# Kernel tuning notes

Measured on AMD Instinct MI355X. Metric: run time of the kernel, lower is better.

The kernel has to match this reference:

```python
import jax, jax.numpy as jnp
import numpy as np

N_NODES = 100000
N_EDGES = 2000000
H = 128


def setup_inputs() -> dict:
    key = jax.random.key(0)
    ks = jax.random.split(key, 5)
    z_src = jax.random.normal(ks[0], (N_NODES, H), dtype=jnp.float32)
    z_dst = jax.random.normal(ks[1], (N_NODES, H), dtype=jnp.float32)
    edge_label_index = jax.random.randint(ks[2], (2, N_EDGES), 0, N_NODES, dtype=jnp.int64)
    # Linear(2H, H) and Linear(H, 1) params (stored as [in, out] for x @ W)
    W1 = jax.random.normal(ks[3], (2 * H, H), dtype=jnp.float32) * (1.0 / np.sqrt(2 * H))
    b1 = jnp.zeros((H,), dtype=jnp.float32)
    W2 = jax.random.normal(ks[4], (H, 1), dtype=jnp.float32) * (1.0 / np.sqrt(H))
    b2 = jnp.zeros((1,), dtype=jnp.float32)
    return {"z_src": z_src, "z_dst": z_dst, "edge_label_index": edge_label_index,
            "W1": W1, "b1": b1, "W2": W2, "b2": b2}


def reference(z_src, z_dst, edge_label_index, W1, b1, W2, b2):
    row, col = edge_label_index[0], edge_label_index[1]
    # gather + concat -> [E, 2H]
    z = jnp.concatenate([z_src[row], z_dst[col]], axis=-1)
    h = jax.nn.relu(z @ W1 + b1)          # [E, H]
    out = h @ W2 + b2                     # [E, 1]
    return out.reshape(-1)
```

## Files before the change

kernel.cpp:

```cpp
#include <hip/hip_runtime.h>

#define HDIM 128

__device__ __forceinline__ unsigned short f2bf_rne(float f) {
    unsigned int u = __float_as_uint(f);
    u += 0x7fffu + ((u >> 16) & 1u);
    return (unsigned short)(u >> 16);
}

__global__ __launch_bounds__(256) void node_gemm_dual(
    const float* __restrict__ Zs, const float* __restrict__ Zd,
    const float* __restrict__ W1, const float* __restrict__ b1,
    unsigned short* __restrict__ Abuf, unsigned short* __restrict__ Bbuf,
    int M, int gb)
{
    __shared__ float zT[128][36];
    __shared__ float ws[64][128];

    const bool second = (blockIdx.x >= gb);
    const float* __restrict__ Z    = second ? Zd : Zs;
    const float* __restrict__ W    = second ? (W1 + HDIM * HDIM) : W1;
    unsigned short* __restrict__ C = second ? Bbuf : Abuf;
    const int bx   = second ? (blockIdx.x - gb) : blockIdx.x;
    const int t    = threadIdx.x;
    const int row0 = bx * 32;

    {
        const int r  = t >> 3;
        const int k0 = (t & 7) << 4;
        int rg = row0 + r;
        if (rg >= M) rg = M - 1;
        const float4* Zv = reinterpret_cast<const float4*>(Z + (size_t)rg * HDIM + k0);
        float4 v0 = Zv[0], v1 = Zv[1], v2 = Zv[2], v3 = Zv[3];
        float vv[16] = {v0.x,v0.y,v0.z,v0.w, v1.x,v1.y,v1.z,v1.w,
                        v2.x,v2.y,v2.z,v2.w, v3.x,v3.y,v3.z,v3.w};
        #pragma unroll
        for (int i = 0; i < 16; ++i) zT[k0 + i][r] = vv[i];
    }

    const int tx = t & 31;
    const int ty = t >> 5;

    float acc[4][4];
    if (second) {
        const float4 bv = *reinterpret_cast<const float4*>(b1 + tx * 4);
        #pragma unroll
        for (int r = 0; r < 4; ++r) {
            acc[r][0] = bv.x; acc[r][1] = bv.y; acc[r][2] = bv.z; acc[r][3] = bv.w;
        }
    } else {
        #pragma unroll
        for (int r = 0; r < 4; ++r)
            #pragma unroll
            for (int c = 0; c < 4; ++c) acc[r][c] = 0.f;
    }

    for (int kk = 0; kk < 128; kk += 64) {
        __syncthreads();
        {
            const float4* Wv = reinterpret_cast<const float4*>(W + (size_t)kk * HDIM);
            float4* Sv = reinterpret_cast<float4*>(&ws[0][0]);
            #pragma unroll
            for (int i = 0; i < 8; ++i) Sv[t + 256 * i] = Wv[t + 256 * i];
        }
        __syncthreads();

        #pragma unroll 8
        for (int k = 0; k < 64; ++k) {
            const float4 zv = *reinterpret_cast<const float4*>(&zT[kk + k][ty * 4]);
            const float4 wv = *reinterpret_cast<const float4*>(&ws[k][tx * 4]);
            acc[0][0] += zv.x * wv.x; acc[0][1] += zv.x * wv.y;
            acc[0][2] += zv.x * wv.z; acc[0][3] += zv.x * wv.w;
            acc[1][0] += zv.y * wv.x; acc[1][1] += zv.y * wv.y;
            acc[1][2] += zv.y * wv.z; acc[1][3] += zv.y * wv.w;
            acc[2][0] += zv.z * wv.x; acc[2][1] += zv.z * wv.y;
            acc[2][2] += zv.z * wv.z; acc[2][3] += zv.z * wv.w;
            acc[3][0] += zv.w * wv.x; acc[3][1] += zv.w * wv.y;
            acc[3][2] += zv.w * wv.z; acc[3][3] += zv.w * wv.w;
        }
    }

    #pragma unroll
    for (int r = 0; r < 4; ++r) {
        const int row = row0 + ty * 4 + r;
        if (row < M) {
            ushort4 o;
            o.x = f2bf_rne(acc[r][0]); o.y = f2bf_rne(acc[r][1]);
            o.z = f2bf_rne(acc[r][2]); o.w = f2bf_rne(acc[r][3]);
            *reinterpret_cast<ushort4*>(C + (size_t)row * HDIM + tx * 4) = o;
        }
    }
}

__global__ __launch_bounds__(256) void edge_decode_bf16(
    const unsigned short* __restrict__ A, const unsigned short* __restrict__ Bm,
    const int* __restrict__ idx,
    const float* __restrict__ W2, const float* __restrict__ b2,
    float* __restrict__ out, int E)
{
    const int t   = threadIdx.x;
    const int sub = t & 15;
    const int grp = t >> 4;

    float w2r[8];
    #pragma unroll
    for (int i = 0; i < 8; ++i) w2r[i] = W2[sub * 8 + i];
    const float b2s = b2[0];

    const int stride = gridDim.x * 16;
    for (int e = blockIdx.x * 16 + grp; e < E; e += stride) {
        const int r = idx[e];
        const int c = idx[E + e];
        const uint4 av = *reinterpret_cast<const uint4*>(A  + (size_t)r * HDIM + sub * 8);
        const uint4 bv = *reinterpret_cast<const uint4*>(Bm + (size_t)c * HDIM + sub * 8);

        float s = 0.f;
        #pragma unroll
        for (int i = 0; i < 4; ++i) {
            const unsigned int ua = (&av.x)[i];
            const unsigned int ub = (&bv.x)[i];
            const float a0 = __uint_as_float(ua << 16);
            const float a1 = __uint_as_float(ua & 0xffff0000u);
            const float b0 = __uint_as_float(ub << 16);
            const float b1v = __uint_as_float(ub & 0xffff0000u);
            s += fmaxf(a0 + b0,  0.f) * w2r[2 * i];
            s += fmaxf(a1 + b1v, 0.f) * w2r[2 * i + 1];
        }
        s += __shfl_xor(s, 1);
        s += __shfl_xor(s, 2);
        s += __shfl_xor(s, 4);
        s += __shfl_xor(s, 8);
        if (sub == 0) out[e] = s + b2s;
    }
}

extern "C" void kernel_launch(void* const* d_in, const int* in_sizes, int n_in,
                              void* d_out, int out_size, void* d_ws, size_t ws_size,
                              hipStream_t stream)
{
    const float* z_src = (const float*)d_in[0];
    const float* z_dst = (const float*)d_in[1];
    const int*   eidx  = (const int*)d_in[2];
    const float* W1    = (const float*)d_in[3];
    const float* b1    = (const float*)d_in[4];
    const float* W2    = (const float*)d_in[5];
    const float* b2    = (const float*)d_in[6];
    float*       outp  = (float*)d_out;

    const int Nn = in_sizes[0] / HDIM;
    const int E  = in_sizes[2] / 2;

    unsigned short* Abuf = (unsigned short*)d_ws;
    unsigned short* Bbuf = Abuf + (size_t)Nn * HDIM;

    const int gb = (Nn + 31) / 32;
    node_gemm_dual<<<2 * gb, 256, 0, stream>>>(z_src, z_dst, W1, b1, Abuf, Bbuf, Nn, gb);
    edge_decode_bf16<<<8192, 256, 0, stream>>>(Abuf, Bbuf, eidx, W2, b2, outp, E);
}
```

Baseline: 339.2 us.

## Use bf16 MFMA for node projection GEMM and unroll edge decode by two

Replaces the fp32 FMA node GEMM with a bf16 MFMA (16x16x32) kernel. A small pre-kernel converts and transposes W1 to bf16, and Z tiles are converted to bf16 in shared memory. The edge decode loop now handles two edges per iteration so more gather loads are in flight. This adds an extra kernel launch and bf16 rounding of the inputs, which lowers precision. The output stores become scalar 2-byte writes that may coalesce poorly.

```diff
diff --git a/kernel.cpp b/kernel.cpp
--- a/kernel.cpp
+++ b/kernel.cpp
@@ -1,93 +1,104 @@
 #include <hip/hip_runtime.h>
 
 #define HDIM 128
+
+typedef __bf16 bf16_t;
+typedef bf16_t bf16x8 __attribute__((ext_vector_type(8)));
+typedef float  f32x4  __attribute__((ext_vector_type(4)));
 
 __device__ __forceinline__ unsigned short f2bf_rne(float f) {
     unsigned int u = __float_as_uint(f);
     u += 0x7fffu + ((u >> 16) & 1u);
     return (unsigned short)(u >> 16);
 }
+__device__ __forceinline__ unsigned int pk_bf2(float a, float b) {
+    return (unsigned int)f2bf_rne(a) | ((unsigned int)f2bf_rne(b) << 16);
+}
 
-__global__ __launch_bounds__(256) void node_gemm_dual(
+__global__ __launch_bounds__(256) void convert_w1(
+    const float* __restrict__ W1, unsigned short* __restrict__ Wt)
+{
+    const int o = blockIdx.x * 256 + threadIdx.x;
+    const int g = o >> 14, rem = o & 16383, n = rem >> 7, k = rem & 127;
+    Wt[o] = f2bf_rne(W1[g * 16384 + k * 128 + n]);
+}
+
+#define ZP 136
+__global__ __launch_bounds__(256) void node_gemm_mfma(
     const float* __restrict__ Zs, const float* __restrict__ Zd,
-    const float* __restrict__ W1, const float* __restrict__ b1,
+    const unsigned short* __restrict__ Wt, const float* __restrict__ b1,
     unsigned short* __restrict__ Abuf, unsigned short* __restrict__ Bbuf,
     int M, int gb)
 {
-    __shared__ float zT[128][36];
-    __shared__ float ws[64][128];
+    __shared__ unsigned short zs[64 * ZP];
+    __shared__ unsigned short wsm[128 * ZP];
 
     const bool second = (blockIdx.x >= gb);
-    const float* __restrict__ Z    = second ? Zd : Zs;
-    const float* __restrict__ W    = second ? (W1 + HDIM * HDIM) : W1;
-    unsigned short* __restrict__ C = second ? Bbuf : Abuf;
+    const float* __restrict__ Z          = second ? Zd : Zs;
+    const unsigned short* __restrict__ W = Wt + (second ? 128 * 128 : 0);
+    unsigned short* __restrict__ C       = second ? Bbuf : Abuf;
     const int bx   = second ? (blockIdx.x - gb) : blockIdx.x;
+    const int row0 = bx * 64;
     const int t    = threadIdx.x;
-    const int row0 = bx * 32;
 
-    {
-        const int r  = t >> 3;
-        const int k0 = (t & 7) << 4;
-        int rg = row0 + r;
-        if (rg >= M) rg = M - 1;
-        const float4* Zv = reinterpret_cast<const float4*>(Z + (size_t)rg * HDIM + k0);
-        float4 v0 = Zv[0], v1 = Zv[1], v2 = Zv[2], v3 = Zv[3];
-        float vv[16] = {v0.x,v0.y,v0.z,v0.w, v1.x,v1.y,v1.z,v1.w,
-                        v2.x,v2.y,v2.z,v2.w, v3.x,v3.y,v3.z,v3.w};
+    #pragma unroll
+    for (int j = 0; j < 8; ++j) {
+        const int u   = t + 256 * j;
+        const int row = u >> 5;
+        const int c4  = u & 31;
+        int rg = row0 + row; if (rg >= M) rg = M - 1;
+        const float4 v = *reinterpret_cast<const float4*>(Z + (size_t)rg * HDIM + c4 * 4);
+        uint2 p; p.x = pk_bf2(v.x, v.y); p.y = pk_bf2(v.z, v.w);
+        *reinterpret_cast<uint2*>(zs + row * ZP + c4 * 4) = p;
+    }
+    #pragma unroll
+    for (int j = 0; j < 8; ++j) {
+        const int u  = t + 256 * j;
+        const int n  = u >> 4;
+        const int k8 = u & 15;
+        const uint4 v = *reinterpret_cast<const uint4*>(W + n * 128 + k8 * 8);
+        *reinterpret_cast<uint4*>(wsm + n * ZP + k8 * 8) = v;
+    }
+    __syncthreads();
+
+    const int lane = t & 63;
+    const int wave = t >> 6;
+    const int m    = lane & 15;
+    const int quad = lane >> 4;
+    const int rw   = wave & 1;
+    const int cw   = wave >> 1;
+
+    const int aoff0 = (rw * 32 +  0 + m) * ZP + quad * 8;
+    const int aoff1 = (rw * 32 + 16 + m) * ZP + quad * 8;
+    const int boff  = (cw * 64 + m) * ZP + quad * 8;
+
+    f32x4 acc[2][4] = {};
+    #pragma unroll
+    for (int ks = 0; ks < 4; ++ks) {
+        const int ko = ks * 32;
+        const bf16x8 a0 = *reinterpret_cast<const bf16x8*>(zs + aoff0 + ko);
+        const bf16x8 a1 = *reinterpret_cast<const bf16x8*>(zs + aoff1 + ko);
         #pragma unroll
-        for (int i = 0; i < 16; ++i) zT[k0 + i][r] = vv[i];
-    }
-
-    const int tx = t & 31;
-    const int ty = t >> 5;
-
-    float acc[4][4];
-    if (second) {
-        const float4 bv = *reinterpret_cast<const float4*>(b1 + tx * 4);
-        #pragma unroll
-        for (int r = 0; r < 4; ++r) {
-            acc[r][0] = bv.x; acc[r][1] = bv.y; acc[r][2] = bv.z; acc[r][3] = bv.w;
-        }
-    } else {
-        #pragma unroll
-        for (int r = 0; r < 4; ++r)
-            #pragma unroll
-            for (int c = 0; c < 4; ++c) acc[r][c] = 0.f;
-    }
-
-    for (int kk = 0; kk < 128; kk += 64) {
-        __syncthreads();
-        {
-            const float4* Wv = reinterpret_cast<const float4*>(W + (size_t)kk * HDIM);
-            float4* Sv = reinterpret_cast<float4*>(&ws[0][0]);
-            #pragma unroll
-            for (int i = 0; i < 8; ++i) Sv[t + 256 * i] = Wv[t + 256 * i];
-        }
-        __syncthreads();
-
-        #pragma unroll 8
-        for (int k = 0; k < 64; ++k) {
-            const float4 zv = *reinterpret_cast<const float4*>(&zT[kk + k][ty * 4]);
-            const float4 wv = *reinterpret_cast<const float4*>(&ws[k][tx * 4]);
-            acc[0][0] += zv.x * wv.x; acc[0][1] += zv.x * wv.y;
-            acc[0][2] += zv.x * wv.z; acc[0][3] += zv.x * wv.w;
-            acc[1][0] += zv.y * wv.x; acc[1][1] += zv.y * wv.y;
-            acc[1][2] += zv.y * wv.z; acc[1][3] += zv.y * wv.w;
-            acc[2][0] += zv.z * wv.x; acc[2][1] += zv.z * wv.y;
-            acc[2][2] += zv.z * wv.z; acc[2][3] += zv.z * wv.w;
-            acc[3][0] += zv.w * wv.x; acc[3][1] += zv.w * wv.y;
-            acc[3][2] += zv.w * wv.z; acc[3][3] += zv.w * wv.w;
+        for (int ct = 0; ct < 4; ++ct) {
+            const bf16x8 bb = *reinterpret_cast<const bf16x8*>(wsm + boff + ct * 16 * ZP + ko);
+            acc[0][ct] = __builtin_amdgcn_mfma_f32_16x16x32_bf16(a0, bb, acc[0][ct], 0, 0, 0);
+            acc[1][ct] = __builtin_amdgcn_mfma_f32_16x16x32_bf16(a1, bb, acc[1][ct], 0, 0, 0);
         }
     }
 
+    const int colbase = cw * 64 + m;
     #pragma unroll
-    for (int r = 0; r < 4; ++r) {
-        const int row = row0 + ty * 4 + r;
-        if (row < M) {
-            ushort4 o;
-            o.x = f2bf_rne(acc[r][0]); o.y = f2bf_rne(acc[r][1]);
-            o.z = f2bf_rne(acc[r][2]); o.w = f2bf_rne(acc[r][3]);
-            *reinterpret_cast<ushort4*>(C + (size_t)row * HDIM + tx * 4) = o;
+    for (int ct = 0; ct < 4; ++ct) {
+        const int col = colbase + ct * 16;
+        const float bv = second ? b1[col] : 0.f;
+        #pragma unroll
+        for (int rt = 0; rt < 2; ++rt) {
+            #pragma unroll
+            for (int i = 0; i < 4; ++i) {
+                const int gr = row0 + rw * 32 + rt * 16 + quad * 4 + i;
+                if (gr < M)
+                    C[(size_t)gr * HDIM + col] = f2bf_rne(acc[rt][ct][i] + bv);
+            }
         }
     }
 }
@@ -107,30 +118,39 @@
     for (int i = 0; i < 8; ++i) w2r[i] = W2[sub * 8 + i];
     const float b2s = b2[0];
 
-    const int stride = gridDim.x * 16;
-    for (int e = blockIdx.x * 16 + grp; e < E; e += stride) {
-        const int r = idx[e];
-        const int c = idx[E + e];
-        const uint4 av = *reinterpret_cast<const uint4*>(A  + (size_t)r * HDIM + sub * 8);
-        const uint4 bv = *reinterpret_cast<const uint4*>(Bm + (size_t)c * HDIM + sub * 8);
+    const int G = gridDim.x * 16;
+    for (int e0 = blockIdx.x * 16 + grp; e0 < E; e0 += 2 * G) {
+        const int  e1 = e0 + G;
+        const bool h1 = (e1 < E);
+        const int r0 = idx[e0];
+        const int c0 = idx[E + e0];
+        const int r1 = h1 ? idx[e1]     : r0;
+        const int c1 = h1 ? idx[E + e1] : c0;
 
-        float s = 0.f;
+        const uint4 a0 = *reinterpret_cast<const uint4*>(A  + (size_t)r0 * HDIM + sub * 8);
+        const uint4 b0 = *reinterpret_cast<const uint4*>(Bm + (size_t)c0 * HDIM + sub * 8);
+        const uint4 a1 = *reinterpret_cast<const uint4*>(A  + (size_t)r1 * HDIM + sub * 8);
+        const uint4 b1v = *reinterpret_cast<const uint4*>(Bm + (size_t)c1 * HDIM + sub * 8);
+
+        float s0 = 0.f, s1 = 0.f;
         #pragma unroll
         for (int i = 0; i < 4; ++i) {
-            const unsigned int ua = (&av.x)[i];
-            const unsigned int ub = (&bv.x)[i];
-            const float a0 = __uint_as_float(ua << 16);
-            const float a1 = __uint_as_float(ua & 0xffff0000u);
-            const float b0 = __uint_as_float(ub << 16);
-            const float b1v = __uint_as_float(ub & 0xffff0000u);
-            s += fmaxf(a0 + b0,  0.f) * w2r[2 * i];
-            s += fmaxf(a1 + b1v, 0.f) * w2r[2 * i + 1];
+            unsigned int ua = (&a0.x)[i], ub = (&b0.x)[i];
+            s0 += fmaxf(__uint_as_float(ua << 16)        + __uint_as_float(ub << 16),        0.f) * w2r[2 * i];
+            s0 += fmaxf(__uint_as_float(ua & 0xffff0000u) + __uint_as_float(ub & 0xffff0000u), 0.f) * w2r[2 * i + 1];
+            unsigned int uc = (&a1.x)[i], ud = (&b1v.x)[i];
+            s1 += fmaxf(__uint_as_float(uc << 16)        + __uint_as_float(ud << 16),        0.f) * w2r[2 * i];
+            s1 += fmaxf(__uint_as_float(uc & 0xffff0000u) + __uint_as_float(ud & 0xffff0000u), 0.f) * w2r[2 * i + 1];
         }
-        s += __shfl_xor(s, 1);
-        s += __shfl_xor(s, 2);
-        s += __shfl_xor(s, 4);
-        s += __shfl_xor(s, 8);
-        if (sub == 0) out[e] = s + b2s;
+        #pragma unroll
+        for (int d = 1; d < 16; d <<= 1) {
+            s0 += __shfl_xor(s0, d);
+            s1 += __shfl_xor(s1, d);
+        }
+        if (sub == 0) {
+            out[e0] = s0 + b2s;
+            if (h1) out[e1] = s1 + b2s;
+        }
     }
 }
 
@@ -152,8 +172,12 @@
 
     unsigned short* Abuf = (unsigned short*)d_ws;
     unsigned short* Bbuf = Abuf + (size_t)Nn * HDIM;
+    unsigned short* Wt   = Bbuf + (size_t)Nn * HDIM;
 
-    const int gb = (Nn + 31) / 32;
-    node_gemm_dual<<<2 * gb, 256, 0, stream>>>(z_src, z_dst, W1, b1, Abuf, Bbuf, Nn, gb);
+    convert_w1<<<128, 256, 0, stream>>>(W1, Wt);
+
+    const int gb = (Nn + 63) / 64;
+    node_gemm_mfma<<<2 * gb, 256, 0, stream>>>(z_src, z_dst, Wt, b1, Abuf, Bbuf, Nn, gb);
+
     edge_decode_bf16<<<8192, 256, 0, stream>>>(Abuf, Bbuf, eidx, W2, b2, outp, E);
 }
```

After: 296.3 us. 12.7% less time.
